# Kernel tuning notes

Hardware: AMD Instinct MI355X
Metric: run time of the kernel (lower is better)

## Reference

```python
import jax, jax.numpy as jnp
from jax import lax
import numpy as np

B, T, D, H = 2048, 512, 16, 48


def _lstm_layer(x, W_ih, W_hh, b_ih, b_hh):
    """Single-layer LSTM, batch_first. x: [B,T,Din] -> hs: [B,T,H].
    PyTorch gate order: i, f, g, o."""
    h_dim = W_hh.shape[1]
    # Precompute input contribution for all timesteps: [B,T,4H]
    xg = jnp.einsum('btd,gd->btg', x, W_ih) + b_ih + b_hh
    xg = jnp.swapaxes(xg, 0, 1)  # [T,B,4H]

    def step(carry, xg_t):
        h, c = carry
        gates = xg_t + h @ W_hh.T  # [B,4H]
        i, f, g, o = jnp.split(gates, 4, axis=-1)
        i = jax.nn.sigmoid(i)
        f = jax.nn.sigmoid(f)
        g = jnp.tanh(g)
        o = jax.nn.sigmoid(o)
        c = f * c + i * g
        h = o * jnp.tanh(c)
        return (h, c), h

    bsz = x.shape[0]
    init = (jnp.zeros((bsz, h_dim), x.dtype), jnp.zeros((bsz, h_dim), x.dtype))
    _, hs = lax.scan(step, init, xg)
    return jnp.swapaxes(hs, 0, 1)  # [B,T,H]


def setup_inputs() -> dict:
    key = jax.random.key(0)
    ks = jax.random.split(key, 11)
    s_in = 1.0 / np.sqrt(H)
    return {
        'x': jax.random.normal(ks[0], (B, T, D), jnp.float32),
        'W_ih0': jax.random.normal(ks[1], (4 * H, D), jnp.float32) * s_in,
        'W_hh0': jax.random.normal(ks[2], (4 * H, H), jnp.float32) * s_in,
        'b_ih0': jax.random.normal(ks[3], (4 * H,), jnp.float32) * s_in,
        'b_hh0': jax.random.normal(ks[4], (4 * H,), jnp.float32) * s_in,
        'W_ih1': jax.random.normal(ks[5], (4 * H, H), jnp.float32) * s_in,
        'W_hh1': jax.random.normal(ks[6], (4 * H, H), jnp.float32) * s_in,
        'b_ih1': jax.random.normal(ks[7], (4 * H,), jnp.float32) * s_in,
        'b_hh1': jax.random.normal(ks[8], (4 * H,), jnp.float32) * s_in,
        'fc_w': jax.random.normal(ks[9], (1, H), jnp.float32) * s_in,
        'fc_b': jax.random.normal(ks[10], (1,), jnp.float32) * s_in,
    }


def reference(x, W_ih0, W_hh0, b_ih0, b_hh0, W_ih1, W_hh1, b_ih1, b_hh1, fc_w, fc_b):
    # 2-layer LSTM (eval mode: inter-layer dropout is identity)
    h1 = _lstm_layer(x, W_ih0, W_hh0, b_ih0, b_hh0)   # [B,T,H]
    h2 = _lstm_layer(h1, W_ih1, W_hh1, b_ih1, b_hh1)  # [B,T,H]
    last = h2[:, -1, :]                               # [B,H]
    logits = last @ fc_w.T + fc_b                     # [B,1]
    return jax.nn.sigmoid(logits)
```

## Files before the change

kernel.cpp:

```cpp
#include <hip/hip_runtime.h>

#define TT 512
#define DD 16
#define HH 48
#define BT 8
#define NTHR 768

typedef short bf8v __attribute__((ext_vector_type(8)));
typedef float f32x4 __attribute__((ext_vector_type(4)));

__device__ __forceinline__ ushort bfb(float f) {
    return __builtin_bit_cast(ushort, (__bf16)f);
}

__device__ __forceinline__ float actf(float x, float A, float M, float Bc) {
    float e = __builtin_amdgcn_exp2f(M * x);
    return __builtin_fmaf(A, __builtin_amdgcn_rcpf(1.0f + e), Bc);
}

__device__ __forceinline__ void barrier_lds() {
    asm volatile("s_waitcnt lgkmcnt(0)\ns_barrier" ::: "memory");
}

__global__ __launch_bounds__(NTHR)
void lstm_kernel(const float* __restrict__ x,
                 const float* __restrict__ Wih0, const float* __restrict__ Whh0,
                 const float* __restrict__ bih0, const float* __restrict__ bhh0,
                 const float* __restrict__ Wih1, const float* __restrict__ Whh1,
                 const float* __restrict__ bih1, const float* __restrict__ bhh1,
                 const float* __restrict__ fcw, const float* __restrict__ fcb,
                 float* __restrict__ out)
{
    __shared__ alignas(16) ushort A0u[2][1024];
    __shared__ alignas(16) ushort A1u[2][1536];
    __shared__ float outl[BT][HH];

    const int tid  = threadIdx.x;
    const int lane = tid & 63;
    const int wave = tid >> 6;
    const int b0   = blockIdx.x * BT;

    const int colq = lane & 15;
    const int quad = lane >> 4;
    const int u    = wave * 4 + quad;
    const bool lo  = (colq < 8);

    const int af_o = quad * 128 + colq * 8;
    const int waddrA1 = lo
        ? ((u >> 3) * 128 + (colq + 8) * 8 + (u & 7))
        : (((48 + u) >> 3) * 128 + colq * 8 + ((48 + u) & 7));
    const int wA0 = ((16 + u) >> 3) * 128 + colq * 8 + ((16 + u) & 7);

    const float L2E = 1.4426950408889634f;

    f32x4 bias0, bias1;
#pragma unroll
    for (int r = 0; r < 4; ++r) {
        bias0[r] = bih0[r * 48 + u] + bhh0[r * 48 + u];
        bias1[r] = bih1[r * 48 + u] + bhh1[r * 48 + u];
    }

    const int gi = (colq & 3) * 48 + wave * 4 + (colq >> 2);
    bf8v w0f0, w0f1, w1f0, w1f1, w1f2;
    {
        bf8v w;
#pragma unroll
        for (int j = 0; j < 8; ++j) {
            int k = quad * 8 + j;
            float v = (k < 16) ? Wih0[gi * 16 + k] : Whh0[gi * 48 + (k - 16)];
            w[j] = (short)bfb(v);
        }
        w0f0 = w;
#pragma unroll
        for (int j = 0; j < 8; ++j) {
            int k = 32 + quad * 8 + j;
            w[j] = (short)bfb(Whh0[gi * 48 + (k - 16)]);
        }
        w0f1 = w;
#pragma unroll
        for (int j = 0; j < 8; ++j) {
            int k = quad * 8 + j;
            w[j] = (short)bfb(Wih1[gi * 48 + k]);
        }
        w1f0 = w;
#pragma unroll
        for (int j = 0; j < 8; ++j) {
            int k = 32 + quad * 8 + j;
            float v = (k < 48) ? Wih1[gi * 48 + k] : Whh1[gi * 48 + (k - 48)];
            w[j] = (short)bfb(v);
        }
        w1f1 = w;
#pragma unroll
        for (int j = 0; j < 8; ++j) {
            int k = 64 + quad * 8 + j;
            w[j] = (short)bfb(Whh1[gi * 48 + (k - 48)]);
        }
        w1f2 = w;
    }

    const bool stg  = (wave >= 10);
    const int  srow = (wave - 10) * 4 + quad;
    const int  sd   = colq;
    const int  sdst = (sd >> 3) * 128 + srow * 8 + (sd & 7);
    const float* sptr = x + (size_t)(b0 + srow) * TT * DD + sd;

    {
        uint* p0 = (uint*)A0u;
        for (int i = tid; i < 1024; i += NTHR) p0[i] = 0;
        uint* p1 = (uint*)A1u;
        for (int i = tid; i < 1536; i += NTHR) p1[i] = 0;
    }
    float r0 = 0.f, r1 = 0.f;
    __syncthreads();
    if (stg) {
        float v = sptr[0];
        r0 = sptr[DD];
        r1 = sptr[2 * DD];
        A0u[0][sdst] = bfb(v);
    }
    __syncthreads();

    float c = 0.f;

#define BODY(P, DOL1, t) { \
        if (stg) { \
            asm volatile("s_waitcnt vmcnt(0)" ::: "memory"); \
            A0u[(P)^1][sdst] = bfb(r0); \
            r0 = r1; \
            int t3 = (t) + 3; if (t3 > TT - 1) t3 = TT - 1; \
            r1 = sptr[t3 * DD]; \
        } \
        bf8v a0 = *(const bf8v*)&A0u[P][af_o]; \
        bf8v a1 = *(const bf8v*)&A0u[P][512 + af_o]; \
        f32x4 acc0 = __builtin_amdgcn_mfma_f32_16x16x32_bf16(w0f0, a0, bias0, 0, 0, 0); \
        acc0 = __builtin_amdgcn_mfma_f32_16x16x32_bf16(w0f1, a1, acc0, 0, 0, 0); \
        f32x4 pre; \
        if (DOL1) { \
            bf8v g0 = *(const bf8v*)&A1u[(P)^1][af_o]; \
            bf8v g1 = *(const bf8v*)&A1u[(P)^1][512 + af_o]; \
            bf8v g2 = *(const bf8v*)&A1u[(P)^1][1024 + af_o]; \
            f32x4 acc1 = __builtin_amdgcn_mfma_f32_16x16x32_bf16(w1f0, g0, bias1, 0, 0, 0); \
            acc1 = __builtin_amdgcn_mfma_f32_16x16x32_bf16(w1f1, g1, acc1, 0, 0, 0); \
            acc1 = __builtin_amdgcn_mfma_f32_16x16x32_bf16(w1f2, g2, acc1, 0, 0, 0); \
            pre[0] = lo ? acc0[0] : acc1[0]; \
            pre[1] = lo ? acc0[1] : acc1[1]; \
            pre[2] = lo ? acc0[2] : acc1[2]; \
            pre[3] = lo ? acc0[3] : acc1[3]; \
        } else { \
            pre = acc0; \
        } \
        float iv = actf(pre[0], 1.0f, -L2E, 0.0f); \
        float fv = actf(pre[1], 1.0f, -L2E, 0.0f); \
        float gv = actf(pre[2], 2.0f, -2.0f * L2E, -1.0f); \
        float ov = actf(pre[3], 1.0f, -L2E, 0.0f); \
        float cn = __builtin_fmaf(fv, c, iv * gv); \
        if (!DOL1) cn = lo ? cn : c;    \
        c = cn; \
        float tc = actf(cn, 2.0f, -2.0f * L2E, -1.0f); \
        hv = ov * tc; \
        ushort hb = bfb(hv); \
        if (DOL1) { A1u[P][waddrA1] = hb; } \
        else if (lo) { A1u[P][waddrA1] = hb; } \
        if (lo) A0u[(P)^1][wA0] = hb; \
        barrier_lds(); \
    }

    float hv = 0.f;
    BODY(0, false, 0)
    for (int t = 1; t < TT - 1; t += 2) {
        BODY(1, true, t)
        BODY(0, true, t + 1)
    }
    BODY(1, true, TT - 1)

    {
        bf8v g0 = *(const bf8v*)&A1u[1][af_o];
        bf8v g1 = *(const bf8v*)&A1u[1][512 + af_o];
        bf8v g2 = *(const bf8v*)&A1u[1][1024 + af_o];
        f32x4 acc1 = __builtin_amdgcn_mfma_f32_16x16x32_bf16(w1f0, g0, bias1, 0, 0, 0);
        acc1 = __builtin_amdgcn_mfma_f32_16x16x32_bf16(w1f1, g1, acc1, 0, 0, 0);
        acc1 = __builtin_amdgcn_mfma_f32_16x16x32_bf16(w1f2, g2, acc1, 0, 0, 0);
        float iv = actf(acc1[0], 1.0f, -L2E, 0.0f);
        float fv = actf(acc1[1], 1.0f, -L2E, 0.0f);
        float gv = actf(acc1[2], 2.0f, -2.0f * L2E, -1.0f);
        float ov = actf(acc1[3], 1.0f, -L2E, 0.0f);
        float cn = __builtin_fmaf(fv, c, iv * gv);
        float tc = actf(cn, 2.0f, -2.0f * L2E, -1.0f);
        hv = ov * tc;
    }

    if (!lo) outl[colq - 8][u] = hv;
    __syncthreads();
    if (tid < BT) {
        float s = fcb[0];
        for (int uu = 0; uu < HH; ++uu) s = __builtin_fmaf(outl[tid][uu], fcw[uu], s);
        out[b0 + tid] = actf(s, 1.0f, -L2E, 0.0f);
    }
#undef BODY
}

extern "C" void kernel_launch(void* const* d_in, const int* in_sizes, int n_in,
                              void* d_out, int out_size, void* d_ws, size_t ws_size,
                              hipStream_t stream) {
    const float* x    = (const float*)d_in[0];
    const float* Wih0 = (const float*)d_in[1];
    const float* Whh0 = (const float*)d_in[2];
    const float* bih0 = (const float*)d_in[3];
    const float* bhh0 = (const float*)d_in[4];
    const float* Wih1 = (const float*)d_in[5];
    const float* Whh1 = (const float*)d_in[6];
    const float* bih1 = (const float*)d_in[7];
    const float* bhh1 = (const float*)d_in[8];
    const float* fcw  = (const float*)d_in[9];
    const float* fcb  = (const float*)d_in[10];
    lstm_kernel<<<2048 / BT, NTHR, 0, stream>>>(x, Wih0, Whh0, bih0, bhh0,
                                                Wih1, Whh1, bih1, bhh1, fcw, fcb,
                                                (float*)d_out);
}
```

Measured before the change: 308.9 us.

## Stage x in 64-step LDS chunks instead of per-step register prefetch

```diff
diff --git a/kernel.cpp b/kernel.cpp
--- a/kernel.cpp
+++ b/kernel.cpp
@@ -5,6 +5,11 @@
 #define HH 48
 #define BT 8
 #define NTHR 768
+#define CHUNK 64
+
+#define XA0H 16384
+#define XA1  17920
+#define STOT 20992
 
 typedef short bf8v __attribute__((ext_vector_type(8)));
 typedef float f32x4 __attribute__((ext_vector_type(4)));
@@ -31,8 +36,7 @@
                  const float* __restrict__ fcw, const float* __restrict__ fcb,
                  float* __restrict__ out)
 {
-    __shared__ alignas(16) ushort A0u[2][1024];
-    __shared__ alignas(16) ushort A1u[2][1536];
+    __shared__ alignas(16) ushort S[STOT];
     __shared__ float outl[BT][HH];
 
     const int tid  = threadIdx.x;
@@ -45,13 +49,21 @@
     const int u    = wave * 4 + quad;
     const bool lo  = (colq < 8);
 
-    const int af_o = quad * 128 + colq * 8;
-    const int waddrA1 = lo
-        ? ((u >> 3) * 128 + (colq + 8) * 8 + (u & 7))
-        : (((48 + u) >> 3) * 128 + colq * 8 + ((48 + u) & 7));
-    const int wA0 = ((16 + u) >> 3) * 128 + colq * 8 + ((16 + u) & 7);
-
     const float L2E = 1.4426950408889634f;
+
+    const int fb = colq * 8;
+    const int inc01 = (quad < 2) ? 2 * 256 : 0;
+    const int a1e = XA0H + (2 + quad) * 128 + fb;
+    const int a1o = a1e + 768;
+    const int g0e = XA1 + 1536 + quad * 128 + fb;
+    const int g0o = g0e - 1536;
+    const int w0  = (u >> 3) * 128 + fb + (u & 7);
+    const int wA0e = XA0H + 768 + w0;
+    const int wA0o = XA0H + w0;
+    const int wr = lo ? ((u >> 3) * 128 + (colq + 8) * 8 + (u & 7))
+                      : (((48 + u) >> 3) * 128 + colq * 8 + ((48 + u) & 7));
+    const int wA1e = XA1 + wr;
+    const int wA1o = XA1 + 1536 + wr;
 
     f32x4 bias0, bias1;
 #pragma unroll
@@ -98,47 +110,25 @@
         w1f2 = w;
     }
 
-    const bool stg  = (wave >= 10);
-    const int  srow = (wave - 10) * 4 + quad;
-    const int  sd   = colq;
-    const int  sdst = (sd >> 3) * 128 + srow * 8 + (sd & 7);
-    const float* sptr = x + (size_t)(b0 + srow) * TT * DD + sd;
-
     {
-        uint* p0 = (uint*)A0u;
-        for (int i = tid; i < 1024; i += NTHR) p0[i] = 0;
-        uint* p1 = (uint*)A1u;
-        for (int i = tid; i < 1536; i += NTHR) p1[i] = 0;
-    }
-    float r0 = 0.f, r1 = 0.f;
+        uint* p = (uint*)S;
+        for (int i = tid; i < STOT / 2; i += NTHR) p[i] = 0;
+    }
     __syncthreads();
-    if (stg) {
-        float v = sptr[0];
-        r0 = sptr[DD];
-        r1 = sptr[2 * DD];
-        A0u[0][sdst] = bfb(v);
-    }
-    __syncthreads();
 
     float c = 0.f;
-
-#define BODY(P, DOL1, t) { \
-        if (stg) { \
-            asm volatile("s_waitcnt vmcnt(0)" ::: "memory"); \
-            A0u[(P)^1][sdst] = bfb(r0); \
-            r0 = r1; \
-            int t3 = (t) + 3; if (t3 > TT - 1) t3 = TT - 1; \
-            r1 = sptr[t3 * DD]; \
-        } \
-        bf8v a0 = *(const bf8v*)&A0u[P][af_o]; \
-        bf8v a1 = *(const bf8v*)&A0u[P][512 + af_o]; \
+    float hv = 0.f;
+
+#define BODY(A0OFF, A1OFF, G0OFF, WA0OFF, WA1OFF, DOL1) { \
+        bf8v a0 = *(const bf8v*)&S[A0OFF]; \
+        bf8v a1 = *(const bf8v*)&S[A1OFF]; \
         f32x4 acc0 = __builtin_amdgcn_mfma_f32_16x16x32_bf16(w0f0, a0, bias0, 0, 0, 0); \
         acc0 = __builtin_amdgcn_mfma_f32_16x16x32_bf16(w0f1, a1, acc0, 0, 0, 0); \
         f32x4 pre; \
         if (DOL1) { \
-            bf8v g0 = *(const bf8v*)&A1u[(P)^1][af_o]; \
-            bf8v g1 = *(const bf8v*)&A1u[(P)^1][512 + af_o]; \
-            bf8v g2 = *(const bf8v*)&A1u[(P)^1][1024 + af_o]; \
+            bf8v g0 = *(const bf8v*)&S[G0OFF]; \
+            bf8v g1 = *(const bf8v*)&S[(G0OFF) + 512]; \
+            bf8v g2 = *(const bf8v*)&S[(G0OFF) + 1024]; \
             f32x4 acc1 = __builtin_amdgcn_mfma_f32_16x16x32_bf16(w1f0, g0, bias1, 0, 0, 0); \
             acc1 = __builtin_amdgcn_mfma_f32_16x16x32_bf16(w1f1, g1, acc1, 0, 0, 0); \
             acc1 = __builtin_amdgcn_mfma_f32_16x16x32_bf16(w1f2, g2, acc1, 0, 0, 0); \
@@ -159,24 +149,46 @@
         float tc = actf(cn, 2.0f, -2.0f * L2E, -1.0f); \
         hv = ov * tc; \
         ushort hb = bfb(hv); \
-        if (DOL1) { A1u[P][waddrA1] = hb; } \
-        else if (lo) { A1u[P][waddrA1] = hb; } \
-        if (lo) A0u[(P)^1][wA0] = hb; \
+        if (DOL1) { S[WA1OFF] = hb; } \
+        else if (lo) { S[WA1OFF] = hb; } \
+        if (lo) S[WA0OFF] = hb; \
         barrier_lds(); \
     }
 
-    float hv = 0.f;
-    BODY(0, false, 0)
-    for (int t = 1; t < TT - 1; t += 2) {
-        BODY(1, true, t)
-        BODY(0, true, t + 1)
-    }
-    BODY(1, true, TT - 1)
+    for (int ck = 0; ck < TT / CHUNK; ++ck) {
+        for (int i = tid; i < BT * CHUNK * 4; i += NTHR) {
+            int g  = i & 3;
+            int tl = (i >> 2) & (CHUNK - 1);
+            int b  = i >> 8;
+            const float4 v = *(const float4*)(x +
+                ((size_t)(b0 + b) * TT + (ck * CHUNK + tl)) * DD + g * 4);
+            ushort4 s4;
+            s4.x = bfb(v.x); s4.y = bfb(v.y); s4.z = bfb(v.z); s4.w = bfb(v.w);
+            *(ushort4*)&S[tl * 256 + (g >> 1) * 128 + b * 8 + (g & 1) * 4] = s4;
+        }
+        __syncthreads();
+
+        int ae = (quad < 2) ? (quad * 128 + fb) : (XA0H + (quad - 2) * 128 + fb);
+        int ao = (quad < 2) ? (256 + quad * 128 + fb) : (XA0H + 768 + (quad - 2) * 128 + fb);
+
+        int p0 = 0;
+        if (ck == 0) {
+            BODY(ae, a1e, g0e, wA0e, wA1e, false)
+            BODY(ao, a1o, g0o, wA0o, wA1o, true)
+            ae += inc01; ao += inc01;
+            p0 = 1;
+        }
+        for (int p = p0; p < CHUNK / 2; ++p) {
+            BODY(ae, a1e, g0e, wA0e, wA1e, true)
+            BODY(ao, a1o, g0o, wA0o, wA1o, true)
+            ae += inc01; ao += inc01;
+        }
+    }
 
     {
-        bf8v g0 = *(const bf8v*)&A1u[1][af_o];
-        bf8v g1 = *(const bf8v*)&A1u[1][512 + af_o];
-        bf8v g2 = *(const bf8v*)&A1u[1][1024 + af_o];
+        bf8v g0 = *(const bf8v*)&S[g0e];
+        bf8v g1 = *(const bf8v*)&S[g0e + 512];
+        bf8v g2 = *(const bf8v*)&S[g0e + 1024];
         f32x4 acc1 = __builtin_amdgcn_mfma_f32_16x16x32_bf16(w1f0, g0, bias1, 0, 0, 0);
         acc1 = __builtin_amdgcn_mfma_f32_16x16x32_bf16(w1f1, g1, acc1, 0, 0, 0);
         acc1 = __builtin_amdgcn_mfma_f32_16x16x32_bf16(w1f2, g2, acc1, 0, 0, 0);
```

New measurement: 307.7 us. About the same (-0.4%).
